# Kernel tuning notes

Measured on AMD Instinct MI355X. Metric: run time of the kernel, lower is better.

Reference implementation:

```python
import jax, jax.numpy as jnp
import numpy as np

DIM_GATE = 256
DIM_BIAS = 128
H = 8
D = 32
EPS = 1e-5


def _layernorm(t, gamma, beta):
    mu = jnp.mean(t, axis=-1, keepdims=True)
    var = jnp.mean(jnp.square(t - mu), axis=-1, keepdims=True)
    return (t - mu) * jax.lax.rsqrt(var + EPS) * gamma + beta


def setup_inputs() -> dict:
    key = jax.random.key(0)
    ks = jax.random.split(key, 12)
    b, l = 2, 512
    x = jax.random.normal(ks[0], (b, l, DIM_GATE), dtype=jnp.float32)
    bias = jax.random.normal(ks[1], (b, l, l, DIM_BIAS), dtype=jnp.float32)
    s_g = 1.0 / np.sqrt(DIM_GATE)
    s_b = 1.0 / np.sqrt(DIM_BIAS)
    return {
        "x": x,
        "bias": bias,
        "g_gamma": jnp.ones((DIM_GATE,), jnp.float32),
        "g_beta": jnp.zeros((DIM_GATE,), jnp.float32),
        "b_gamma": jnp.ones((DIM_BIAS,), jnp.float32),
        "b_beta": jnp.zeros((DIM_BIAS,), jnp.float32),
        "Wq": jax.random.normal(ks[2], (DIM_GATE, H * D), jnp.float32) * s_g,
        "Wk": jax.random.normal(ks[3], (DIM_GATE, H * D), jnp.float32) * s_g,
        "Wv": jax.random.normal(ks[4], (DIM_GATE, H * D), jnp.float32) * s_g,
        "Wb": jax.random.normal(ks[5], (DIM_BIAS, H), jnp.float32) * s_b,
        "Wg": jax.random.normal(ks[6], (DIM_GATE, H * D), jnp.float32) * s_g,
        "bg": jnp.zeros((H * D,), jnp.float32),
        "Wout": jax.random.normal(ks[7], (H * D, DIM_GATE), jnp.float32) * s_g,
        "bout": jnp.zeros((DIM_GATE,), jnp.float32),
    }


def reference(x, bias, g_gamma, g_beta, b_gamma, b_beta, Wq, Wk, Wv, Wb, Wg, bg, Wout, bout):
    b, l, _ = x.shape
    scaling = 1.0 / np.sqrt(D)
    xn = _layernorm(x, g_gamma, g_beta)                      # [b,l,dg]
    bn = _layernorm(bias, b_gamma, b_beta)                   # [b,l,l,db]
    q = (xn @ Wq).reshape(b, l, H, D)                        # [b,l,h,d]
    k = (xn @ Wk).reshape(b, l, H, D) * scaling
    v = (xn @ Wv).reshape(b, l, H, D)
    pair_b = bn @ Wb                                         # [b,q,k,h]
    gate = jax.nn.sigmoid(xn @ Wg + bg)                      # [b,l,h*d]
    attn = jnp.einsum('bqhd,bkhd->bqkh', q, k) + pair_b      # [b,q,k,h]
    attn = jax.nn.softmax(attn, axis=-2)                     # softmax over k
    out = jnp.einsum('bqkh,bkhd->bqhd', attn, v).reshape(b, l, H * D)
    out = gate * out
    return out @ Wout + bout
```

## Files before the change

kernel.cpp:

```cpp
#include <hip/hip_runtime.h>
#include <math.h>

#define LSEQ 512
#define DG 256
#define DB 128
#define NH 8
#define HD 32
#define EPSV 1e-5f
#define LP2 516

typedef __attribute__((ext_vector_type(8))) short bf16x8;
typedef __attribute__((ext_vector_type(4))) float f32x4;

__device__ __forceinline__ unsigned short f2bf(float x) {
    unsigned int u = __float_as_uint(x);
    u += 0x7FFFu + ((u >> 16) & 1u);
    return (unsigned short)(u >> 16);
}
__device__ __forceinline__ float bf2f(unsigned short h) {
    return __uint_as_float(((unsigned int)h) << 16);
}

__global__ __launch_bounds__(256) void prep_kernel(
    const float* __restrict__ x, const float* __restrict__ g_gamma,
    const float* __restrict__ g_beta, const float* __restrict__ Wq,
    const float* __restrict__ Wk, const float* __restrict__ Wv,
    const float* __restrict__ Wg, const float* __restrict__ bg,
    float* __restrict__ q_ws, float* __restrict__ k_ws,
    float* __restrict__ v_ws, float* __restrict__ g_ws)
{
    __shared__ float xs[4][DG];
    const int t = threadIdx.x;
    const int wave = t >> 6, lane = t & 63;
    const int row0 = blockIdx.x << 2;

    {
        const int row = row0 + wave;
        const float4 xv = *(const float4*)(x + (size_t)row * DG + lane * 4);
        float s  = xv.x + xv.y + xv.z + xv.w;
        float ss = xv.x*xv.x + xv.y*xv.y + xv.z*xv.z + xv.w*xv.w;
        #pragma unroll
        for (int m = 32; m >= 1; m >>= 1) { s += __shfl_xor(s, m); ss += __shfl_xor(ss, m); }
        const float mean = s * (1.f / DG);
        const float rstd = rsqrtf(ss * (1.f / DG) - mean * mean + EPSV);
        const float4 gg = *(const float4*)(g_gamma + lane * 4);
        const float4 gb = *(const float4*)(g_beta + lane * 4);
        float4 xo;
        xo.x = (xv.x - mean) * rstd * gg.x + gb.x;
        xo.y = (xv.y - mean) * rstd * gg.y + gb.y;
        xo.z = (xv.z - mean) * rstd * gg.z + gb.z;
        xo.w = (xv.w - mean) * rstd * gg.w + gb.w;
        *(float4*)&xs[wave][lane * 4] = xo;
    }
    __syncthreads();

    float aq[4] = {0,0,0,0}, ak[4] = {0,0,0,0}, av[4] = {0,0,0,0}, ag[4] = {0,0,0,0};
    #pragma unroll 4
    for (int c = 0; c < DG; ++c) {
        const float wq = Wq[(size_t)c * DG + t];
        const float wk = Wk[(size_t)c * DG + t];
        const float wv = Wv[(size_t)c * DG + t];
        const float wg = Wg[(size_t)c * DG + t];
        #pragma unroll
        for (int r = 0; r < 4; ++r) {
            const float xr = xs[r][c];
            aq[r] = fmaf(xr, wq, aq[r]);
            ak[r] = fmaf(xr, wk, ak[r]);
            av[r] = fmaf(xr, wv, av[r]);
            ag[r] = fmaf(xr, wg, ag[r]);
        }
    }

    const float scal = 0.17677669529663687f;
    const float bgv = bg[t];
    #pragma unroll
    for (int r = 0; r < 4; ++r) {
        const size_t o = (size_t)(row0 + r) * DG + t;
        q_ws[o] = aq[r];
        k_ws[o] = ak[r] * scal;
        v_ws[o] = av[r];
        g_ws[o] = 1.f / (1.f + __expf(-(ag[r] + bgv)));
    }
}

__global__ __launch_bounds__(256) void pairb_kernel(
    const float* __restrict__ bias, const float* __restrict__ b_gamma,
    const float* __restrict__ b_beta, const float* __restrict__ Wb,
    float* __restrict__ pair_ws)
{
    __shared__ float lds[4 * 2 * 2048];
    const int t = threadIdx.x;
    const int w = t >> 6, l = t & 63;
    const int n = l & 15, quad = l >> 4;
    const int bq = blockIdx.x;

    bf16x8 gwhi[4], gwlo[4];
    float S1 = 0.f, S0 = 0.f;
    #pragma unroll
    for (int ks = 0; ks < 4; ++ks) {
        #pragma unroll
        for (int j = 0; j < 8; ++j) {
            const int c = ks * 32 + quad * 8 + j;
            const float wb = (n < 8) ? Wb[c * 8 + n] : 0.f;
            const float wv = b_gamma[c] * wb;
            S1 += wv;
            S0 += b_beta[c] * wb;
            unsigned short hi = f2bf(wv);
            unsigned short lo = f2bf(wv - bf2f(hi));
            if (n == 8) { hi = 0x3F80; lo = 0; }
            gwhi[ks][j] = (short)hi;
            gwlo[ks][j] = (short)lo;
        }
    }
    S1 += __shfl_xor(S1, 16); S1 += __shfl_xor(S1, 32);
    S0 += __shfl_xor(S0, 16); S0 += __shfl_xor(S0, 32);

    float* myl = lds + w * 4096;
    const size_t rowbase = (size_t)bq * LSEQ + w * 16;

    auto stage = [&](int tt, int buf) {
        const float* src = bias + (rowbase + (size_t)tt * 64) * DB;
        float* dst = myl + buf * 2048;
        #pragma unroll
        for (int i = 0; i < 8; ++i) {
            __builtin_amdgcn_global_load_lds(
                (const __attribute__((address_space(1))) void*)(src + i * 256 + l * 4),
                (__attribute__((address_space(3))) void*)(dst + i * 256 + l * 4),
                16, 0, 0);
        }
    };

    auto compute = [&](int tt, int buf) {
        const float* d = myl + buf * 2048 + n * 128 + quad * 8;
        f32x4 acc = {0.f, 0.f, 0.f, 0.f};
        float ssq = 0.f;
        #pragma unroll
        for (int ks = 0; ks < 4; ++ks) {
            const float4 x0 = *(const float4*)(d + ks * 32);
            const float4 x1 = *(const float4*)(d + ks * 32 + 4);
            ssq = fmaf(x0.x,x0.x, fmaf(x0.y,x0.y, fmaf(x0.z,x0.z, fmaf(x0.w,x0.w, ssq))));
            ssq = fmaf(x1.x,x1.x, fmaf(x1.y,x1.y, fmaf(x1.z,x1.z, fmaf(x1.w,x1.w, ssq))));
            const float xsv[8] = {x0.x,x0.y,x0.z,x0.w,x1.x,x1.y,x1.z,x1.w};
            bf16x8 ahi, alo;
            #pragma unroll
            for (int j = 0; j < 8; ++j) {
                const unsigned short hi = f2bf(xsv[j]);
                ahi[j] = (short)hi;
                alo[j] = (short)f2bf(xsv[j] - bf2f(hi));
            }
            acc = __builtin_amdgcn_mfma_f32_16x16x32_bf16(ahi, gwhi[ks], acc, 0, 0, 0);
            acc = __builtin_amdgcn_mfma_f32_16x16x32_bf16(alo, gwhi[ks], acc, 0, 0, 0);
            acc = __builtin_amdgcn_mfma_f32_16x16x32_bf16(ahi, gwlo[ks], acc, 0, 0, 0);
        }
        ssq += __shfl_xor(ssq, 16);
        ssq += __shfl_xor(ssq, 32);
        float* pout = pair_ws + (rowbase + (size_t)tt * 64 + quad * 4) * NH + n;
        #pragma unroll
        for (int reg = 0; reg < 4; ++reg) {
            const float sumr = __uint_as_float((unsigned)__builtin_amdgcn_ds_bpermute(
                (quad * 16 + 8) * 4, (int)__float_as_uint(acc[reg])));
            const float ssqr = __uint_as_float((unsigned)__builtin_amdgcn_ds_bpermute(
                (quad * 4 + reg) * 4, (int)__float_as_uint(ssq)));
            const float mean = sumr * (1.f / DB);
            const float var  = ssqr * (1.f / DB) - mean * mean;
            const float rstd = rsqrtf(var + EPSV);
            const float p = rstd * (acc[reg] - mean * S1) + S0;
            if (n < NH) pout[reg * NH] = p;
        }
    };

    stage(0, 0);
    stage(1, 1);
    asm volatile("s_waitcnt vmcnt(8)" ::: "memory");
    compute(0, 0);
    for (int tt = 1; tt < 7; ++tt) {
        stage(tt + 1, (tt + 1) & 1);
        asm volatile("s_waitcnt vmcnt(12)" ::: "memory");
        compute(tt, tt & 1);
    }
    asm volatile("s_waitcnt vmcnt(4)" ::: "memory");
    compute(7, 1);
}

__global__ __launch_bounds__(512) void attn_kernel(
    const float* __restrict__ pair_ws, const float* __restrict__ Wout,
    const float* __restrict__ bout, const float* __restrict__ q_ws,
    const float* __restrict__ k_ws, const float* __restrict__ v_ws,
    const float* __restrict__ g_ws, float* __restrict__ out)
{
    __shared__ float lg[2 * NH * LP2];
    __shared__ float q_s[2 * DG];
    __shared__ float ps[4 * 2 * 64 * 4];
    __shared__ float row_s[2 * DG];
    __shared__ float rden[16];

    const int t = threadIdx.x;
    const int b = blockIdx.x >> 8;
    const int q0 = (blockIdx.x & 255) * 2;

    {
        const float* pbase = pair_ws + ((size_t)(b * LSEQ + q0)) * LSEQ * NH;
        #pragma unroll
        for (int r = 0; r < 4; ++r) {
            const int f = r * 512 + t;
            const float4 pv = *(const float4*)(pbase + (size_t)f * 4);
            const int q = f >> 10;
            const int o = (f * 4) & 4095;
            const int k = o >> 3, hb = o & 7;
            float* dst = lg + (q * NH + hb) * LP2 + k;
            dst[0] = pv.x; dst[LP2] = pv.y; dst[2*LP2] = pv.z; dst[3*LP2] = pv.w;
        }
        q_s[t] = q_ws[((size_t)(b * LSEQ + q0)) * DG + t];
    }
    __syncthreads();

    {
        const int h = t >> 6, kk = t & 63;
        const float* kb = k_ws + ((size_t)(b * LSEQ)) * DG + h * HD;
        const float* qp0 = q_s + h * HD;
        const float* qp1 = q_s + DG + h * HD;
        for (int j = 0; j < 8; ++j) {
            const int k = kk + j * 64;
            const float* kr = kb + (size_t)k * DG;
            float a0 = 0.f, a1 = 0.f;
            #pragma unroll
            for (int c = 0; c < 8; ++c) {
                const float4 kv = *(const float4*)(kr + c * 4);
                const float4 qa = *(const float4*)(qp0 + c * 4);
                const float4 qb = *(const float4*)(qp1 + c * 4);
                a0 = fmaf(kv.x, qa.x, fmaf(kv.y, qa.y, fmaf(kv.z, qa.z, fmaf(kv.w, qa.w, a0))));
                a1 = fmaf(kv.x, qb.x, fmaf(kv.y, qb.y, fmaf(kv.z, qb.z, fmaf(kv.w, qb.w, a1))));
            }
            lg[(0 * NH + h) * LP2 + k] += a0;
            lg[(1 * NH + h) * LP2 + k] += a1;
        }
    }
    __syncthreads();

    {
        const int qh = t >> 5, l32 = t & 31;
        float* lrow = lg + qh * LP2;
        float mx = -1e30f;
        #pragma unroll
        for (int i = 0; i < 16; ++i) mx = fmaxf(mx, lrow[l32 + i * 32]);
        #pragma unroll
        for (int m = 16; m >= 1; m >>= 1) mx = fmaxf(mx, __shfl_xor(mx, m));
        float s = 0.f;
        #pragma unroll
        for (int i = 0; i < 16; ++i) {
            const int k = l32 + i * 32;
            const float e = __expf(lrow[k] - mx);
            lrow[k] = e;
            s += e;
        }
        #pragma unroll
        for (int m = 16; m >= 1; m >>= 1) s += __shfl_xor(s, m);
        if (l32 == 0) rden[qh] = 1.f / s;
    }
    __syncthreads();

    {
        const int q = t >> 8, s4 = (t >> 6) & 3, c4 = t & 63;
        const int h = c4 >> 3;
        const float* vb = v_ws + ((size_t)(b * LSEQ + s4 * 128)) * DG + c4 * 4;
        const float* prow = lg + (q * NH + h) * LP2 + s4 * 128;
        float4 a = {0.f, 0.f, 0.f, 0.f};
        #pragma unroll 4
        for (int i = 0; i < 128; ++i) {
            const float p = prow[i];
            const float4 vv = *(const float4*)(vb + (size_t)i * DG);
            a.x = fmaf(p, vv.x, a.x);
            a.y = fmaf(p, vv.y, a.y);
            a.z = fmaf(p, vv.z, a.z);
            a.w = fmaf(p, vv.w, a.w);
        }
        *(float4*)&ps[((s4 * 2 + q) * 64 + c4) * 4] = a;
    }
    __syncthreads();
    if (t < 128) {
        const int q = t >> 6, c4 = t & 63, h = c4 >> 3;
        float4 a = *(const float4*)&ps[((0 * 2 + q) * 64 + c4) * 4];
        #pragma unroll
        for (int s4 = 1; s4 < 4; ++s4) {
            const float4 p4 = *(const float4*)&ps[((s4 * 2 + q) * 64 + c4) * 4];
            a.x += p4.x; a.y += p4.y; a.z += p4.z; a.w += p4.w;
        }
        const float sc = rden[q * NH + h];
        const float4 g4 = *(const float4*)(g_ws + ((size_t)(b * LSEQ + q0 + q)) * DG + c4 * 4);
        float* rs = row_s + q * DG + c4 * 4;
        rs[0] = a.x * sc * g4.x;
        rs[1] = a.y * sc * g4.y;
        rs[2] = a.z * sc * g4.z;
        rs[3] = a.w * sc * g4.w;
    }
    __syncthreads();

    {
        const int q = t >> 8, co = t & 255;
        const float* rs = row_s + q * DG;
        const float* wo = Wout + co;
        float a = 0.f;
        #pragma unroll 4
        for (int c = 0; c < DG; ++c)
            a = fmaf(rs[c], wo[(size_t)c * DG], a);
        out[((size_t)(b * LSEQ + q0 + q)) * DG + co] = a + bout[co];
    }
}

extern "C" void kernel_launch(void* const* d_in, const int* in_sizes, int n_in,
                              void* d_out, int out_size, void* d_ws, size_t ws_size,
                              hipStream_t stream)
{
    const float* x       = (const float*)d_in[0];
    const float* bias    = (const float*)d_in[1];
    const float* g_gamma = (const float*)d_in[2];
    const float* g_beta  = (const float*)d_in[3];
    const float* b_gamma = (const float*)d_in[4];
    const float* b_beta  = (const float*)d_in[5];
    const float* Wq      = (const float*)d_in[6];
    const float* Wk      = (const float*)d_in[7];
    const float* Wv      = (const float*)d_in[8];
    const float* Wb      = (const float*)d_in[9];
    const float* Wg      = (const float*)d_in[10];
    const float* bg      = (const float*)d_in[11];
    const float* Wout    = (const float*)d_in[12];
    const float* bout    = (const float*)d_in[13];
    float* out = (float*)d_out;

    float* ws      = (float*)d_ws;
    float* q_ws    = ws;
    float* k_ws    = ws + 262144;
    float* v_ws    = ws + 2 * 262144;
    float* g_ws    = ws + 3 * 262144;
    float* pair_ws = ws + 4 * 262144;

    hipLaunchKernelGGL(prep_kernel, dim3(256), dim3(256), 0, stream,
                       x, g_gamma, g_beta, Wq, Wk, Wv, Wg, bg,
                       q_ws, k_ws, v_ws, g_ws);
    hipLaunchKernelGGL(pairb_kernel, dim3(1024), dim3(256), 0, stream,
                       bias, b_gamma, b_beta, Wb, pair_ws);
    hipLaunchKernelGGL(attn_kernel, dim3(512), dim3(512), 0, stream,
                       pair_ws, Wout, bout, q_ws, k_ws, v_ws, g_ws, out);
}
```

Baseline: 534.8 us.

## Stage K tiles in LDS via direct loads and share V loads across queries

The QK logits stage now copies 64-row chunks of K into padded LDS with global_load_lds and keeps q in registers, so each wave reads its head slice from LDS instead of making strided per-thread global loads. The PV stage is restructured so each thread accumulates both query rows from a single V load, splitting the keys into 8 segments, with a wider LDS reduction afterwards. The goal is less redundant global traffic for K and V. In exchange it adds about 66KB of LDS and two barriers per chunk, which could lower occupancy.

```diff
diff --git a/kernel.cpp b/kernel.cpp
--- a/kernel.cpp
+++ b/kernel.cpp
@@ -8,6 +8,7 @@
 #define HD 32
 #define EPSV 1e-5f
 #define LP2 516
+#define KPAD 257
 
 typedef __attribute__((ext_vector_type(8))) short bf16x8;
 typedef __attribute__((ext_vector_type(4))) float f32x4;
@@ -189,12 +190,14 @@
     const float* __restrict__ g_ws, float* __restrict__ out)
 {
     __shared__ float lg[2 * NH * LP2];
+    __shared__ float ks_lds[64 * KPAD];
     __shared__ float q_s[2 * DG];
-    __shared__ float ps[4 * 2 * 64 * 4];
+    __shared__ float ps[8][2][DG];
     __shared__ float row_s[2 * DG];
     __shared__ float rden[16];
 
     const int t = threadIdx.x;
+    const int w = t >> 6, l = t & 63;
     const int b = blockIdx.x >> 8;
     const int q0 = (blockIdx.x & 255) * 2;
 
@@ -215,27 +218,45 @@
     __syncthreads();
 
     {
-        const int h = t >> 6, kk = t & 63;
-        const float* kb = k_ws + ((size_t)(b * LSEQ)) * DG + h * HD;
-        const float* qp0 = q_s + h * HD;
-        const float* qp1 = q_s + DG + h * HD;
+        float qr0[32], qr1[32];
+        #pragma unroll
         for (int j = 0; j < 8; ++j) {
-            const int k = kk + j * 64;
-            const float* kr = kb + (size_t)k * DG;
+            const float4 a = *(const float4*)&q_s[w * HD + j * 4];
+            const float4 c = *(const float4*)&q_s[DG + w * HD + j * 4];
+            qr0[j*4+0]=a.x; qr0[j*4+1]=a.y; qr0[j*4+2]=a.z; qr0[j*4+3]=a.w;
+            qr1[j*4+0]=c.x; qr1[j*4+1]=c.y; qr1[j*4+2]=c.z; qr1[j*4+3]=c.w;
+        }
+        const float* kbase = k_ws + (size_t)(b * LSEQ) * DG;
+
+        for (int ch = 0; ch < 8; ++ch) {
+            #pragma unroll
+            for (int i = 0; i < 8; ++i) {
+                const int row = i * 8 + w;
+                const float* src = kbase + (size_t)(ch * 64 + row) * DG;
+                float* dst = ks_lds + row * KPAD;
+                __builtin_amdgcn_global_load_lds(
+                    (const __attribute__((address_space(1))) void*)(src + l * 4),
+                    (__attribute__((address_space(3))) void*)(dst + l * 4),
+                    16, 0, 0);
+            }
+            __syncthreads();
+
+            const float* kr = ks_lds + l * KPAD + w * HD;
             float a0 = 0.f, a1 = 0.f;
             #pragma unroll
-            for (int c = 0; c < 8; ++c) {
-                const float4 kv = *(const float4*)(kr + c * 4);
-                const float4 qa = *(const float4*)(qp0 + c * 4);
-                const float4 qb = *(const float4*)(qp1 + c * 4);
-                a0 = fmaf(kv.x, qa.x, fmaf(kv.y, qa.y, fmaf(kv.z, qa.z, fmaf(kv.w, qa.w, a0))));
-                a1 = fmaf(kv.x, qb.x, fmaf(kv.y, qb.y, fmaf(kv.z, qb.z, fmaf(kv.w, qb.w, a1))));
+            for (int j = 0; j < 8; ++j) {
+                const float4 kv = *(const float4*)(kr + j * 4);
+                a0 = fmaf(kv.x, qr0[j*4+0], fmaf(kv.y, qr0[j*4+1],
+                     fmaf(kv.z, qr0[j*4+2], fmaf(kv.w, qr0[j*4+3], a0))));
+                a1 = fmaf(kv.x, qr1[j*4+0], fmaf(kv.y, qr1[j*4+1],
+                     fmaf(kv.z, qr1[j*4+2], fmaf(kv.w, qr1[j*4+3], a1))));
             }
-            lg[(0 * NH + h) * LP2 + k] += a0;
-            lg[(1 * NH + h) * LP2 + k] += a1;
-        }
-    }
-    __syncthreads();
+            const int kidx = ch * 64 + l;
+            lg[(0 * NH + w) * LP2 + kidx] += a0;
+            lg[(1 * NH + w) * LP2 + kidx] += a1;
+            __syncthreads();
+        }
+    }
 
     {
         const int qh = t >> 5, l32 = t & 31;
@@ -260,38 +281,38 @@
     __syncthreads();
 
     {
-        const int q = t >> 8, s4 = (t >> 6) & 3, c4 = t & 63;
-        const int h = c4 >> 3;
-        const float* vb = v_ws + ((size_t)(b * LSEQ + s4 * 128)) * DG + c4 * 4;
-        const float* prow = lg + (q * NH + h) * LP2 + s4 * 128;
-        float4 a = {0.f, 0.f, 0.f, 0.f};
-        #pragma unroll 4
-        for (int i = 0; i < 128; ++i) {
-            const float p = prow[i];
-            const float4 vv = *(const float4*)(vb + (size_t)i * DG);
-            a.x = fmaf(p, vv.x, a.x);
-            a.y = fmaf(p, vv.y, a.y);
-            a.z = fmaf(p, vv.z, a.z);
-            a.w = fmaf(p, vv.w, a.w);
-        }
-        *(float4*)&ps[((s4 * 2 + q) * 64 + c4) * 4] = a;
-    }
-    __syncthreads();
-    if (t < 128) {
-        const int q = t >> 6, c4 = t & 63, h = c4 >> 3;
-        float4 a = *(const float4*)&ps[((0 * 2 + q) * 64 + c4) * 4];
-        #pragma unroll
-        for (int s4 = 1; s4 < 4; ++s4) {
-            const float4 p4 = *(const float4*)&ps[((s4 * 2 + q) * 64 + c4) * 4];
-            a.x += p4.x; a.y += p4.y; a.z += p4.z; a.w += p4.w;
-        }
-        const float sc = rden[q * NH + h];
-        const float4 g4 = *(const float4*)(g_ws + ((size_t)(b * LSEQ + q0 + q)) * DG + c4 * 4);
-        float* rs = row_s + q * DG + c4 * 4;
-        rs[0] = a.x * sc * g4.x;
-        rs[1] = a.y * sc * g4.y;
-        rs[2] = a.z * sc * g4.z;
-        rs[3] = a.w * sc * g4.w;
+        const int s8 = t >> 6, c4 = t & 63, h = c4 >> 3;
+        const float* vb = v_ws + ((size_t)(b * LSEQ + s8 * 64)) * DG + c4 * 4;
+        const float* p0 = lg + (0 * NH + h) * LP2 + s8 * 64;
+        const float* p1 = lg + (1 * NH + h) * LP2 + s8 * 64;
+        float4 A0 = {0,0,0,0}, A1 = {0,0,0,0};
+        #pragma unroll 2
+        for (int i = 0; i < 64; i += 4) {
+            const float4 pa = *(const float4*)(p0 + i);
+            const float4 pb = *(const float4*)(p1 + i);
+            #pragma unroll
+            for (int r = 0; r < 4; ++r) {
+                const float4 vv = *(const float4*)(vb + (size_t)(i + r) * DG);
+                const float wa = (r == 0) ? pa.x : (r == 1) ? pa.y : (r == 2) ? pa.z : pa.w;
+                const float wb2 = (r == 0) ? pb.x : (r == 1) ? pb.y : (r == 2) ? pb.z : pb.w;
+                A0.x = fmaf(wa, vv.x, A0.x);  A0.y = fmaf(wa, vv.y, A0.y);
+                A0.z = fmaf(wa, vv.z, A0.z);  A0.w = fmaf(wa, vv.w, A0.w);
+                A1.x = fmaf(wb2, vv.x, A1.x); A1.y = fmaf(wb2, vv.y, A1.y);
+                A1.z = fmaf(wb2, vv.z, A1.z); A1.w = fmaf(wb2, vv.w, A1.w);
+            }
+        }
+        *(float4*)&ps[s8][0][c4 * 4] = A0;
+        *(float4*)&ps[s8][1][c4 * 4] = A1;
+    }
+    __syncthreads();
+    {
+        const int q = t >> 8, c = t & 255;
+        float a = ps[0][q][c];
+        #pragma unroll
+        for (int s8 = 1; s8 < 8; ++s8) a += ps[s8][q][c];
+        const float sc = rden[q * NH + (c >> 5)];
+        const float g = g_ws[((size_t)(b * LSEQ + q0 + q)) * DG + c];
+        row_s[q * DG + c] = a * sc * g;
     }
     __syncthreads();
 
```

Result: no change. 536.2 us (+0.3%).
